# Kernel optimization log

Hardware: AMD Instinct MI355X
Metric: run time of the kernel (lower is better)

Reference implementation:

```python
import jax, jax.numpy as jnp
import numpy as np

B, D, F_UP, F_DOWN, C = 4096, 768, 12288, 12288, 256


def setup_inputs() -> dict:
    key = jax.random.key(0)
    ks = jax.random.split(key, 12)
    s = np.float32(1.0 / np.sqrt(D))
    return {
        'initial_acts': jax.random.normal(ks[0], (B, D), jnp.float32),
        'x_up': jax.random.normal(ks[1], (B, D), jnp.float32),
        'ln_scale': jax.random.uniform(ks[2], (B,), jnp.float32) + 0.5,
        'W_enc_up': jax.random.normal(ks[3], (F_UP, D), jnp.float32) * s,
        'b_enc_up': jax.random.normal(ks[4], (F_UP,), jnp.float32) * 0.01,
        'b_dec_up': jax.random.normal(ks[5], (D,), jnp.float32) * 0.01,
        'W_dec_up': jax.random.normal(ks[6], (D, F_UP), jnp.float32) * s,
        'W_enc_down': jax.random.normal(ks[7], (F_DOWN, D), jnp.float32) * s,
        'b_enc_down': jax.random.normal(ks[8], (F_DOWN,), jnp.float32) * 0.01,
        'b_dec_down': jax.random.normal(ks[9], (D,), jnp.float32) * 0.01,
        'W_dec_down': jax.random.normal(ks[10], (D, F_DOWN), jnp.float32) * s,
        'connections': jax.random.randint(ks[11], (F_DOWN, C), 0, F_UP, jnp.int64),
        'k_up': 64,
        'k_down': 64,
    }


def _topk_sparse(pre, k):
    # pre: [B, F] -> keep top-k per row, zeros elsewhere
    vals, idx = jax.lax.top_k(pre, k)
    rows = jnp.arange(pre.shape[0])[:, None]
    return jnp.zeros_like(pre).at[rows, idx].set(vals)


def _topk_encode(x, W_enc, b_enc, b_dec, k):
    # AutoEncoderTopK.encode: relu(encoder(x - b_dec)), then top-k sparsify
    pre = jax.nn.relu((x - b_dec) @ W_enc.T + b_enc)
    return _topk_sparse(pre, k)


def reference(initial_acts, x_up, ln_scale, W_enc_up, b_enc_up, b_dec_up,
              W_dec_up, W_enc_down, b_enc_down, b_dec_down, W_dec_down,
              connections, k_up, k_down):
    f_down, f_up = W_enc_down.shape[0], W_enc_up.shape[0]
    # upstream features (vanilla_forward -> features[up_name])
    feat_up = _topk_encode(x_up, W_enc_up, b_enc_up, b_dec_up, k_up)  # [B, F_up]
    # connection mask [F_down, F_up] from index tensor
    rows = jnp.arange(f_down)[:, None]
    mask = jnp.zeros((f_down, f_up), jnp.bool_).at[rows, connections].set(True)
    # get_pruned_contributions: masked virtual-weight matmul
    virtual_w = (W_enc_down @ W_dec_up) * mask                        # [F_down, F_up]
    contributions = feat_up @ virtual_w.T + (W_enc_down @ b_dec_up)   # [B, F_down]
    # get_initial_contributions + accumulate
    approx = initial_acts @ W_enc_down.T + contributions
    # layernorm scale, encoder bias, b_dec correction
    approx = approx / ln_scale[:, None] + b_enc_down - (W_enc_down @ b_dec_down)
    # downstream TopK + decode
    feat_down = _topk_sparse(approx, k_down)                          # [B, F_down]
    recon = feat_down @ W_dec_down.T + b_dec_down                     # [B, D]
    return recon
```

## Files before the change

kernel.cpp:

```cpp
#include <hip/hip_runtime.h>
#include <stdint.h>

#define B_    4096
#define D_    768
#define FUP   12288
#define FDN   12288
#define CONN  256
#define KTOP  64
#define CHUNK 1024
#define NCH   (B_ / CHUNK)
#define CH2   512
#define NCH2  (B_ / CH2)
#define PDW   1024
#define NPW   (FUP / PDW)

typedef short short8v __attribute__((ext_vector_type(8)));
typedef float f32x4  __attribute__((ext_vector_type(4)));


__device__ __forceinline__ unsigned fkey(float x) {
    unsigned u = __float_as_uint(x);
    return (u & 0x80000000u) ? ~u : (u | 0x80000000u);
}

__device__ void topk64_block(const float* vals, int n, int* gidx, float* gval,
                             unsigned* hist, int* scratch)
{
    const int tid = threadIdx.x;
    if (tid == 0) { scratch[0] = KTOP; scratch[1] = 0; scratch[2] = 0; scratch[3] = 0; }
    for (int l = 24; l >= 0; l -= 8) {
        hist[tid] = 0;
        __syncthreads();
        unsigned prefix = (unsigned)scratch[1];
        unsigned hm = (l == 24) ? 0u : (0xFFFFFFFFu << (l + 8));
        for (int i = tid; i < n; i += 256) {
            unsigned key = fkey(vals[i]);
            if ((key & hm) == (prefix & hm)) atomicAdd(&hist[(key >> l) & 255], 1u);
        }
        __syncthreads();
        if (tid == 0) {
            int need = scratch[0];
            unsigned acc = 0;
            for (int b2 = 255; b2 >= 0; --b2) {
                unsigned h = hist[b2];
                if (acc + h >= (unsigned)need) {
                    scratch[1] = (int)(prefix | ((unsigned)b2 << l));
                    scratch[0] = need - (int)acc;
                    break;
                }
                acc += h;
            }
        }
        __syncthreads();
    }
    unsigned thresh = (unsigned)scratch[1];
    for (int i = tid; i < n; i += 256) {
        float v = vals[i];
        unsigned key = fkey(v);
        if (key > thresh) {
            int p = atomicAdd(&scratch[2], 1);
            gidx[p] = i; gval[p] = v;
        } else if (key == thresh) {
            int p = atomicAdd(&scratch[3], 1);
            if (p < 64) scratch[4 + p] = i;
        }
    }
    __syncthreads();
    if (tid == 0) {
        int cnt = scratch[2];
        int ne  = KTOP - cnt;
        int ec  = scratch[3] < 64 ? scratch[3] : 64;
        for (int a2 = 0; a2 < ne; ++a2) {
            int best = 0x7fffffff, bi = -1;
            for (int q = 0; q < ec; ++q) {
                int id = scratch[4 + q];
                if (id >= 0 && id < best) { best = id; bi = q; }
            }
            if (bi >= 0) {
                scratch[4 + bi] = -1;
                gidx[cnt + a2] = best; gval[cnt + a2] = vals[best];
            }
        }
    }
    __syncthreads();
}


__global__ void k_detect(const int* __restrict__ conn, int* mode) {
    if (blockIdx.x == 0 && threadIdx.x == 0) {
        int z = 1;
        for (int i = 1; i < 128; i += 2) z &= (conn[i] == 0);
        *mode = z;
    }
}

__device__ __forceinline__ int getconn(const int* c, size_t e, int mode) {
    return mode ? c[2 * e] : c[e];
}

__global__ void k_zero(unsigned* __restrict__ p, int n) {
    for (int i = blockIdx.x * blockDim.x + threadIdx.x; i < n;
         i += gridDim.x * blockDim.x)
        p[i] = 0u;
}

__global__ void k_transpose(const float* __restrict__ in, float* __restrict__ out,
                            int R, int Cc) {
    __shared__ float t[32][33];
    int x = blockIdx.x * 32 + threadIdx.x;
    int yb = blockIdx.y * 32;
    for (int j = threadIdx.y; j < 32; j += 8)
        t[j][threadIdx.x] = in[(size_t)(yb + j) * Cc + x];
    __syncthreads();
    int xo  = yb + threadIdx.x;
    int yb2 = blockIdx.x * 32;
    for (int j = threadIdx.y; j < 32; j += 8)
        out[(size_t)(yb2 + j) * R + xo] = t[threadIdx.x][j];
}

__global__ void k_precompute(const float* __restrict__ Wup, const float* __restrict__ Wdn,
                             const float* __restrict__ b_enc_up, const float* __restrict__ b_enc_down,
                             const float* __restrict__ b_dec_up, const float* __restrict__ b_dec_down,
                             float* __restrict__ bias_up, float* __restrict__ c_in,
                             float* __restrict__ c_out) {
    int wave = threadIdx.x >> 6, lane = threadIdx.x & 63;
    int f = blockIdx.x * 4 + wave;
    if (f >= FUP) return;
    const float* ru = Wup + (size_t)f * D_;
    const float* rd = Wdn + (size_t)f * D_;
    float s1 = 0.f, s2 = 0.f, s3 = 0.f;
    for (int d = lane; d < D_; d += 64) {
        float bu = b_dec_up[d], bd = b_dec_down[d];
        s1 += ru[d] * bu;
        float w = rd[d];
        s2 += w * bu;
        s3 += w * bd;
    }
    for (int m = 32; m; m >>= 1) {
        s1 += __shfl_xor(s1, m);
        s2 += __shfl_xor(s2, m);
        s3 += __shfl_xor(s3, m);
    }
    if (!lane) {
        bias_up[f] = b_enc_up[f] - s1;
        c_in[f]  = s2;
        c_out[f] = b_enc_down[f] - s3;
    }
}

__device__ __forceinline__ unsigned short bf16rne(float f) {
    unsigned u = __float_as_uint(f);
    unsigned r = u + 0x7FFFu + ((u >> 16) & 1u);
    return (unsigned short)(r >> 16);
}
__global__ __launch_bounds__(256) void k_split3(const float* __restrict__ in,
                                                unsigned short* __restrict__ out,
                                                int R) {
    const size_t plane = (size_t)R * D_;
    size_t base = ((size_t)blockIdx.x * 256 + threadIdx.x) * 8;
    float v[8];
    *(float4*)&v[0] = *(const float4*)(in + base);
    *(float4*)&v[4] = *(const float4*)(in + base + 4);
    unsigned short h[8], m[8], l[8];
#pragma unroll
    for (int i = 0; i < 8; ++i) {
        float f = v[i];
        unsigned short hb = bf16rne(f);
        float hf = __uint_as_float((unsigned)hb << 16);
        float r1 = f - hf;
        unsigned short mb = bf16rne(r1);
        float mf = __uint_as_float((unsigned)mb << 16);
        float r2 = r1 - mf;
        unsigned short lb = bf16rne(r2);
        h[i] = hb; m[i] = mb; l[i] = lb;
    }
    *(short8v*)(out + base)             = *(short8v*)h;
    *(short8v*)(out + plane + base)     = *(short8v*)m;
    *(short8v*)(out + 2 * plane + base) = *(short8v*)l;
}

#define GBM 128
#define GBN 128
#define GBK 32

__device__ __forceinline__ void gld16(const void* g, void* l) {
    __builtin_amdgcn_global_load_lds(
        (const __attribute__((address_space(1))) unsigned int*)g,
        (__attribute__((address_space(3))) unsigned int*)l, 16, 0, 0);
}

__global__ __launch_bounds__(256, 2) void k_gemm_mfma(
    const unsigned short* __restrict__ Asp, const unsigned short* __restrict__ Bsp,
    float* __restrict__ C, const float* __restrict__ bias,
    int M, int N, int doRelu)
{
    __shared__ __attribute__((aligned(16))) unsigned short L[3072 * 8];
    const int tid = threadIdx.x;
    const int nbx = gridDim.x;
    const int nwg = nbx * gridDim.y;
    int id = blockIdx.y * nbx + blockIdx.x;
    if ((nwg & 7) == 0) id = (id & 7) * (nwg >> 3) + (id >> 3);
    const int bm = (id / nbx) * GBM, bn = (id % nbx) * GBN;

    const int wid = tid >> 6, lane = tid & 63;
    const int wm = (wid >> 1) * 64, wn = (wid & 1) * 64;
    const int l15 = lane & 15, g4 = lane >> 4;
    const size_t psA = (size_t)M * D_, psB = (size_t)N * D_;

    const unsigned short* gsrc[12];
    unsigned short* ldst[12];
#pragma unroll
    for (int q2 = 0; q2 < 12; ++q2) {
        int s  = wid * 768 + q2 * 64 + lane;
        int isB = (s >= 1536);
        int sl = isB ? (s - 1536) : s;
        int p  = sl >> 9;
        int rem = sl & 511;
        int r  = rem >> 2;
        int cs = rem & 3;
        int c  = cs ^ ((r >> 1) & 3);
        const unsigned short* bp = isB ? Bsp : Asp;
        size_t ps = isB ? psB : psA;
        int row = (isB ? bn : bm) + r;
        gsrc[q2] = bp + (size_t)p * ps + (size_t)row * D_ + c * 8;
        ldst[q2] = L + (wid * 768 + q2 * 64) * 8;
    }
    const int fA = ((wm + l15) >> 1) & 3;
    const int fB = ((wn + l15) >> 1) & 3;
    const unsigned short* aB = L + (wm + l15) * 32 + ((g4 ^ fA) * 8);
    const unsigned short* bB = L + 1536 * 8 + (wn + l15) * 32 + ((g4 ^ fB) * 8);

    f32x4 acc[4][4] = {};
    for (int k0 = 0; k0 < D_; k0 += GBK) {
        __syncthreads();
#pragma unroll
        for (int q2 = 0; q2 < 12; ++q2)
            gld16(gsrc[q2] + k0, ldst[q2]);
        __syncthreads();
        short8v af[3][4], bf[3][4];
#pragma unroll
        for (int i = 0; i < 4; ++i)
#pragma unroll
            for (int p = 0; p < 3; ++p) {
                af[p][i] = *(const short8v*)(aB + p * 4096 + i * 512);
                bf[p][i] = *(const short8v*)(bB + p * 4096 + i * 512);
            }
#pragma unroll
        for (int i = 0; i < 4; ++i)
#pragma unroll
            for (int j = 0; j < 4; ++j) {
                acc[i][j] = __builtin_amdgcn_mfma_f32_16x16x32_bf16(af[0][i], bf[0][j], acc[i][j], 0, 0, 0);
                acc[i][j] = __builtin_amdgcn_mfma_f32_16x16x32_bf16(af[0][i], bf[1][j], acc[i][j], 0, 0, 0);
                acc[i][j] = __builtin_amdgcn_mfma_f32_16x16x32_bf16(af[1][i], bf[0][j], acc[i][j], 0, 0, 0);
                acc[i][j] = __builtin_amdgcn_mfma_f32_16x16x32_bf16(af[1][i], bf[1][j], acc[i][j], 0, 0, 0);
                acc[i][j] = __builtin_amdgcn_mfma_f32_16x16x32_bf16(af[0][i], bf[2][j], acc[i][j], 0, 0, 0);
                acc[i][j] = __builtin_amdgcn_mfma_f32_16x16x32_bf16(af[2][i], bf[0][j], acc[i][j], 0, 0, 0);
            }
    }
#pragma unroll
    for (int i = 0; i < 4; ++i) {
        int gr0 = bm + wm + i * 16 + (lane >> 4) * 4;
#pragma unroll
        for (int j = 0; j < 4; ++j) {
            int gc = bn + wn + j * 16 + l15;
            float bv = bias ? bias[gc] : 0.f;
#pragma unroll
            for (int q = 0; q < 4; ++q) {
                float v = acc[i][j][q] + bv;
                if (doRelu) v = fmaxf(v, 0.f);
                C[(size_t)(gr0 + q) * N + gc] = v;
            }
        }
    }
}

__global__ __launch_bounds__(256) void k_topk_up(const float* __restrict__ big,
                                                 int* __restrict__ up_idx,
                                                 float* __restrict__ up_val) {
    __shared__ __attribute__((aligned(16))) float row[FUP];
    __shared__ unsigned hist[256];
    __shared__ int scratch[68];
    int b = blockIdx.x;
    const float4* s4 = (const float4*)(big + (size_t)b * FUP);
    float4* r4 = (float4*)row;
    for (int i = threadIdx.x; i < FUP / 4; i += 256) r4[i] = s4[i];
    __syncthreads();
    topk64_block(row, FUP, up_idx + b * 64, up_val + b * 64, hist, scratch);
}

__global__ __launch_bounds__(256) void k_sortwin(
    const int* __restrict__ conn, const int* __restrict__ mode_p,
    unsigned short* __restrict__ ent_fu, unsigned char* __restrict__ ent_c,
    unsigned short* __restrict__ woff)
{
    __shared__ int crow[CONN];
    __shared__ int cnt[NPW + 1];
    __shared__ int base[NPW + 1];
    __shared__ int cur[NPW + 1];
    int fd = blockIdx.x, tid = threadIdx.x;
    int mode = *mode_p;
    crow[tid] = getconn(conn, (size_t)fd * CONN + tid, mode);
    if (tid <= NPW) cnt[tid] = 0;
    __syncthreads();
    int fu = crow[tid];
    bool dup = false;
    for (int q = 0; q < tid; ++q) dup |= (crow[q] == fu);
    int win = dup ? NPW : (fu / PDW);
    atomicAdd(&cnt[win], 1);
    __syncthreads();
    if (tid == 0) {
        int run = 0;
        for (int i = 0; i <= NPW; ++i) { base[i] = run; run += cnt[i]; }
    }
    __syncthreads();
    if (tid <= NPW) {
        woff[fd * (NPW + 2) + tid] = (unsigned short)base[tid];
        cur[tid] = base[tid];
    }
    if (tid == 0) woff[fd * (NPW + 2) + NPW + 1] = (unsigned short)CONN;
    __syncthreads();
    int pos = atomicAdd(&cur[win], 1);
    ent_fu[(size_t)fd * CONN + pos] = (unsigned short)fu;
    ent_c[(size_t)fd * CONN + pos]  = (unsigned char)tid;
}

__global__ __launch_bounds__(256) void k_pd2(
    const float* __restrict__ Wdn, const float* __restrict__ WduT,
    const unsigned short* __restrict__ ent_fu, const unsigned char* __restrict__ ent_c,
    const unsigned short* __restrict__ woff, float* __restrict__ pd)
{
    __shared__ __attribute__((aligned(16))) float wrow[D_];
    int fd = blockIdx.x, win = blockIdx.y, tid = threadIdx.x;
    int s = woff[fd * (NPW + 2) + win];
    int e = woff[fd * (NPW + 2) + win + 1];
    if (win == NPW) {
        for (int t = s + tid; t < e; t += 256)
            pd[(size_t)fd * CONN + ent_c[(size_t)fd * CONN + t]] = 0.f;
        return;
    }
    if (s == e) return;
    const float4* wsrc = (const float4*)(Wdn + (size_t)fd * D_);
    for (int i = tid; i < D_ / 4; i += 256) ((float4*)wrow)[i] = wsrc[i];
    __syncthreads();
    const int wave = tid >> 6, lane = tid & 63;
    const int grp = lane >> 4, gi = lane & 15;
    float4 wr[12];
#pragma unroll
    for (int j = 0; j < 12; ++j)
        wr[j] = *(const float4*)&wrow[gi * 4 + j * 64];
    for (int q = s + wave * 4; q < e; q += 16) {
        int idx = q + grp;
        bool act = idx < e;
        int idxc = act ? idx : (e - 1);
        int fu = ent_fu[(size_t)fd * CONN + idxc];
        const float* wu = WduT + (size_t)fu * D_;
        float sacc = 0.f;
#pragma unroll
        for (int j = 0; j < 12; ++j) {
            float4 u = *(const float4*)&wu[gi * 4 + j * 64];
            sacc = fmaf(u.x, wr[j].x, sacc);
            sacc = fmaf(u.y, wr[j].y, sacc);
            sacc = fmaf(u.z, wr[j].z, sacc);
            sacc = fmaf(u.w, wr[j].w, sacc);
        }
#pragma unroll
        for (int m = 1; m < 16; m <<= 1) sacc += __shfl_xor(sacc, m);
        if (act && gi == 0)
            pd[(size_t)fd * CONN + ent_c[(size_t)fd * CONN + idx]] = sacc;
    }
}

__global__ void k_hist(const int* __restrict__ conn, const int* __restrict__ mode_p,
                       unsigned* __restrict__ counts, int total) {
    int mode = *mode_p;
    for (int e = blockIdx.x * blockDim.x + threadIdx.x; e < total;
         e += gridDim.x * blockDim.x)
        atomicAdd(&counts[getconn(conn, (size_t)e, mode)], 1u);
}

__global__ void k_scan(const unsigned* __restrict__ counts,
                       unsigned* __restrict__ offsets, unsigned* __restrict__ cursor) {
    __shared__ unsigned sums[256];
    int tid = threadIdx.x;
    const int CH = FUP / 256;
    unsigned local = 0;
    for (int i = 0; i < CH; ++i) local += counts[tid * CH + i];
    sums[tid] = local;
    __syncthreads();
    for (int off = 1; off < 256; off <<= 1) {
        unsigned v = 0;
        if (tid >= off) v = sums[tid - off];
        __syncthreads();
        sums[tid] += v;
        __syncthreads();
    }
    unsigned run = (tid == 0) ? 0u : sums[tid - 1];
    for (int i = 0; i < CH; ++i) {
        int idx = tid * CH + i;
        offsets[idx] = run;
        cursor[idx]  = run;
        run += counts[idx];
    }
    if (tid == 255) offsets[FUP] = run;
}

__global__ void k_scatter(const int* __restrict__ conn, const int* __restrict__ mode_p,
                          const float* __restrict__ pd, unsigned* __restrict__ cursor,
                          unsigned short* __restrict__ rev_fd, float* __restrict__ rev_w,
                          int total) {
    int mode = *mode_p;
    for (int e = blockIdx.x * blockDim.x + threadIdx.x; e < total;
         e += gridDim.x * blockDim.x) {
        int fu = getconn(conn, (size_t)e, mode);
        unsigned pos = atomicAdd(&cursor[fu], 1u);
        rev_fd[pos] = (unsigned short)(e >> 8);
        rev_w[pos]  = pd[e];
    }
}

__global__ __launch_bounds__(256) void k_down(
    const float* __restrict__ big , const float* __restrict__ ln_scale,
    const float* __restrict__ c_in, const float* __restrict__ c_out,
    const int* __restrict__ up_idx, const float* __restrict__ up_val,
    const unsigned* __restrict__ offsets, const unsigned short* __restrict__ rev_fd,
    const float* __restrict__ rev_w, int* __restrict__ down_idx,
    float* __restrict__ down_val)
{
    __shared__ __attribute__((aligned(16))) float contrib[FDN];
    __shared__ unsigned hist[256];
    __shared__ int scratch[68];
    int b = blockIdx.x, tid = threadIdx.x;
    float4* c4 = (float4*)contrib;
    for (int i = tid; i < FDN / 4; i += 256) c4[i] = make_float4(0.f, 0.f, 0.f, 0.f);
    __syncthreads();
    for (int j = 0; j < KTOP; ++j) {
        int fu = up_idx[b * 64 + j];
        float v = up_val[b * 64 + j];
        unsigned s = offsets[fu], e = offsets[fu + 1];
        for (unsigned t = s + tid; t < e; t += 256)
            atomicAdd(&contrib[rev_fd[t]], v * rev_w[t]);
    }
    __syncthreads();
    float ls = ln_scale[b];
    const float* ap = big + (size_t)b * FDN;
    for (int i = tid; i < FDN; i += 256)
        contrib[i] = (ap[i] + contrib[i] + c_in[i]) / ls + c_out[i];
    __syncthreads();
    topk64_block(contrib, FDN, down_idx + b * 64, down_val + b * 64, hist, scratch);
}

__global__ __launch_bounds__(256) void k_decode(
    const int* __restrict__ down_idx, const float* __restrict__ down_val,
    const float* __restrict__ WddT, const float* __restrict__ b_dec_down,
    float* __restrict__ out)
{
    __shared__ int fidx[64];
    __shared__ float fval[64];
    int b = blockIdx.x, tid = threadIdx.x;
    if (tid < 64) { fidx[tid] = down_idx[b * 64 + tid]; fval[tid] = down_val[b * 64 + tid]; }
    __syncthreads();
    float a0 = b_dec_down[tid], a1 = b_dec_down[tid + 256], a2 = b_dec_down[tid + 512];
    for (int j = 0; j < 64; ++j) {
        const float* r = WddT + (size_t)fidx[j] * D_;
        float v = fval[j];
        a0 += v * r[tid];
        a1 += v * r[tid + 256];
        a2 += v * r[tid + 512];
    }
    float* o = out + (size_t)b * D_;
    o[tid] = a0; o[tid + 256] = a1; o[tid + 512] = a2;
}


extern "C" void kernel_launch(void* const* d_in, const int* in_sizes, int n_in,
                              void* d_out, int out_size, void* d_ws, size_t ws_size,
                              hipStream_t stream)
{
    const float* initial_acts = (const float*)d_in[0];
    const float* x_up         = (const float*)d_in[1];
    const float* ln_scale     = (const float*)d_in[2];
    const float* W_enc_up     = (const float*)d_in[3];
    const float* b_enc_up     = (const float*)d_in[4];
    const float* b_dec_up     = (const float*)d_in[5];
    const float* W_dec_up     = (const float*)d_in[6];
    const float* W_enc_down   = (const float*)d_in[7];
    const float* b_enc_down   = (const float*)d_in[8];
    const float* b_dec_down   = (const float*)d_in[9];
    const float* W_dec_down   = (const float*)d_in[10];
    const int*   conn         = (const int*)d_in[11];
    float* out = (float*)d_out;

    char* w = (char*)d_ws;
    float*          big      = (float*)(w);
    float*          pd       = (float*)(w);
    unsigned short* ent_fu   = (unsigned short*)(w + 12582912);
    unsigned char*  ent_c    = (unsigned char*) (w + 18874368);
    unsigned short* woff     = (unsigned short*)(w + 22020096);
    unsigned short* Bsplit   = (unsigned short*)(w + 50331648);
    float*          Wt       = (float*)(w + 50331648);
    float*          rev_w    = (float*)(w + 106954752);
    unsigned short* Asplit1  = (unsigned short*)(w + 106954752);
    unsigned short* rev_fd   = (unsigned short*)(w + 119537664);
    unsigned short* Asplit2  = (unsigned short*)(w + 125829120);
    int*            up_idx   = (int*)  (w + 128188416);
    float*          up_val   = (float*)(w + 129236992);
    int*            down_idx = (int*)  (w + 130285568);
    float*          down_val = (float*)(w + 131334144);
    unsigned*       offsets  = (unsigned*)(w + 132382720);
    unsigned*       cursor   = (unsigned*)(w + 132448256);
    unsigned*       counts   = (unsigned*)(w + 132513792);
    float*          bias_up  = (float*)(w + 132579328);
    float*          c_in     = (float*)(w + 132628480);
    float*          c_out    = (float*)(w + 132677632);
    int*            mode_p   = (int*)  (w + 132726784);

    const int total_conn = FDN * CONN;
    dim3 tb(32, 8);

    k_detect<<<1, 64, 0, stream>>>(conn, mode_p);
    k_precompute<<<FUP / 4, 256, 0, stream>>>(W_enc_up, W_enc_down, b_enc_up, b_enc_down,
                                              b_dec_up, b_dec_down, bias_up, c_in, c_out);
    k_split3<<<FUP * D_ / 2048, 256, 0, stream>>>(W_enc_up, Bsplit, FUP);
    for (int c = 0; c < NCH; ++c) {
        k_split3<<<CHUNK * D_ / 2048, 256, 0, stream>>>(x_up + (size_t)c * CHUNK * D_,
                                                        Asplit1, CHUNK);
        k_gemm_mfma<<<dim3(FUP / GBN, CHUNK / GBM), 256, 0, stream>>>(
            Asplit1, Bsplit, big, bias_up, CHUNK, FUP, 1);
        k_topk_up<<<CHUNK, 256, 0, stream>>>(big, up_idx + (size_t)c * CHUNK * 64,
                                             up_val + (size_t)c * CHUNK * 64);
    }
    k_transpose<<<dim3(FUP / 32, D_ / 32), tb, 0, stream>>>(W_dec_up, Wt, D_, FUP);
    k_sortwin<<<FDN, 256, 0, stream>>>(conn, mode_p, ent_fu, ent_c, woff);
    k_pd2<<<dim3(FDN, NPW + 1), 256, 0, stream>>>(W_enc_down, Wt, ent_fu, ent_c, woff, pd);
    k_zero<<<48, 256, 0, stream>>>(counts, FUP);
    k_hist<<<4096, 256, 0, stream>>>(conn, mode_p, counts, total_conn);
    k_scan<<<1, 256, 0, stream>>>(counts, offsets, cursor);
    k_scatter<<<4096, 256, 0, stream>>>(conn, mode_p, pd, cursor, rev_fd, rev_w, total_conn);
    k_split3<<<FDN * D_ / 2048, 256, 0, stream>>>(W_enc_down, Bsplit, FDN);
    for (int c = 0; c < NCH2; ++c) {
        k_split3<<<CH2 * D_ / 2048, 256, 0, stream>>>(initial_acts + (size_t)c * CH2 * D_,
                                                      Asplit2, CH2);
        k_gemm_mfma<<<dim3(FDN / GBN, CH2 / GBM), 256, 0, stream>>>(
            Asplit2, Bsplit, big, nullptr, CH2, FDN, 0);
        k_down<<<CH2, 256, 0, stream>>>(big, ln_scale + (size_t)c * CH2, c_in, c_out,
                                        up_idx + (size_t)c * CH2 * 64,
                                        up_val + (size_t)c * CH2 * 64,
                                        offsets, rev_fd, rev_w,
                                        down_idx + (size_t)c * CH2 * 64,
                                        down_val + (size_t)c * CH2 * 64);
    }
    k_transpose<<<dim3(FDN / 32, D_ / 32), tb, 0, stream>>>(W_dec_down, Wt, D_, FDN);
    k_decode<<<B_, 256, 0, stream>>>(down_idx, down_val, Wt, b_dec_down, out);
}
```

Baseline: 3.886 ms.

## Map one 16-lane group per down-feature in masked virtual-weight kernel

The kernel that computes the pruned virtual weights now gives each 16-lane group its own downstream feature, with 16 features per block, instead of one feature per 256-thread block. Each group reads its W_enc_down row straight from global memory, so the shared-memory staging and __syncthreads go away. All 12 float4 loads of each gathered W_dec_up row are issued before the FMAs, spread over four independent accumulators, to expose more memory-level parallelism. The grid shrinks 16x and far fewer blocks exit early on empty windows. In exchange, lanes within a wave now iterate over windows of different lengths and diverge, and register pressure rises.

Result: slower. 4.042 ms (+4.0%).

```diff
diff --git a/kernel.cpp b/kernel.cpp
--- a/kernel.cpp
+++ b/kernel.cpp
@@ -324,49 +324,53 @@
     ent_c[(size_t)fd * CONN + pos]  = (unsigned char)tid;
 }
 
-__global__ __launch_bounds__(256) void k_pd2(
+__global__ __launch_bounds__(256) void k_pd5(
     const float* __restrict__ Wdn, const float* __restrict__ WduT,
     const unsigned short* __restrict__ ent_fu, const unsigned char* __restrict__ ent_c,
     const unsigned short* __restrict__ woff, float* __restrict__ pd)
 {
-    __shared__ __attribute__((aligned(16))) float wrow[D_];
-    int fd = blockIdx.x, win = blockIdx.y, tid = threadIdx.x;
-    int s = woff[fd * (NPW + 2) + win];
-    int e = woff[fd * (NPW + 2) + win + 1];
+    const int win = blockIdx.y, tid = threadIdx.x;
+    const int grp = tid >> 4, gi = tid & 15;
+    const int fd = blockIdx.x * 16 + grp;
+    const size_t ebase = (size_t)fd * CONN;
     if (win == NPW) {
-        for (int t = s + tid; t < e; t += 256)
-            pd[(size_t)fd * CONN + ent_c[(size_t)fd * CONN + t]] = 0.f;
+        int s = woff[fd * (NPW + 2) + NPW];
+        for (int t = s + gi; t < CONN; t += 16)
+            pd[ebase + ent_c[ebase + t]] = 0.f;
         return;
     }
+    const int s = woff[fd * (NPW + 2) + win];
+    const int e = woff[fd * (NPW + 2) + win + 1];
     if (s == e) return;
-    const float4* wsrc = (const float4*)(Wdn + (size_t)fd * D_);
-    for (int i = tid; i < D_ / 4; i += 256) ((float4*)wrow)[i] = wsrc[i];
-    __syncthreads();
-    const int wave = tid >> 6, lane = tid & 63;
-    const int grp = lane >> 4, gi = lane & 15;
+    const float* wd = Wdn + (size_t)fd * D_;
     float4 wr[12];
 #pragma unroll
     for (int j = 0; j < 12; ++j)
-        wr[j] = *(const float4*)&wrow[gi * 4 + j * 64];
-    for (int q = s + wave * 4; q < e; q += 16) {
-        int idx = q + grp;
-        bool act = idx < e;
-        int idxc = act ? idx : (e - 1);
-        int fu = ent_fu[(size_t)fd * CONN + idxc];
+        wr[j] = *(const float4*)(wd + gi * 4 + j * 64);
+    for (int t = s; t < e; ++t) {
+        int fu = ent_fu[ebase + t];
         const float* wu = WduT + (size_t)fu * D_;
-        float sacc = 0.f;
-#pragma unroll
-        for (int j = 0; j < 12; ++j) {
-            float4 u = *(const float4*)&wu[gi * 4 + j * 64];
-            sacc = fmaf(u.x, wr[j].x, sacc);
-            sacc = fmaf(u.y, wr[j].y, sacc);
-            sacc = fmaf(u.z, wr[j].z, sacc);
-            sacc = fmaf(u.w, wr[j].w, sacc);
+        float4 u[12];
+#pragma unroll
+        for (int j = 0; j < 12; ++j)
+            u[j] = *(const float4*)(wu + gi * 4 + j * 64);
+        float s0 = 0.f, s1 = 0.f, s2 = 0.f, s3 = 0.f;
+#pragma unroll
+        for (int j = 0; j < 12; j += 4) {
+            s0 = fmaf(u[j+0].x, wr[j+0].x, s0); s0 = fmaf(u[j+0].y, wr[j+0].y, s0);
+            s0 = fmaf(u[j+0].z, wr[j+0].z, s0); s0 = fmaf(u[j+0].w, wr[j+0].w, s0);
+            s1 = fmaf(u[j+1].x, wr[j+1].x, s1); s1 = fmaf(u[j+1].y, wr[j+1].y, s1);
+            s1 = fmaf(u[j+1].z, wr[j+1].z, s1); s1 = fmaf(u[j+1].w, wr[j+1].w, s1);
+            s2 = fmaf(u[j+2].x, wr[j+2].x, s2); s2 = fmaf(u[j+2].y, wr[j+2].y, s2);
+            s2 = fmaf(u[j+2].z, wr[j+2].z, s2); s2 = fmaf(u[j+2].w, wr[j+2].w, s2);
+            s3 = fmaf(u[j+3].x, wr[j+3].x, s3); s3 = fmaf(u[j+3].y, wr[j+3].y, s3);
+            s3 = fmaf(u[j+3].z, wr[j+3].z, s3); s3 = fmaf(u[j+3].w, wr[j+3].w, s3);
         }
+        float sacc = (s0 + s1) + (s2 + s3);
 #pragma unroll
         for (int m = 1; m < 16; m <<= 1) sacc += __shfl_xor(sacc, m);
-        if (act && gi == 0)
-            pd[(size_t)fd * CONN + ent_c[(size_t)fd * CONN + idx]] = sacc;
+        if (gi == 0)
+            pd[ebase + ent_c[ebase + t]] = sacc;
     }
 }
 
@@ -531,7 +535,8 @@
     }
     k_transpose<<<dim3(FUP / 32, D_ / 32), tb, 0, stream>>>(W_dec_up, Wt, D_, FUP);
     k_sortwin<<<FDN, 256, 0, stream>>>(conn, mode_p, ent_fu, ent_c, woff);
-    k_pd2<<<dim3(FDN, NPW + 1), 256, 0, stream>>>(W_enc_down, Wt, ent_fu, ent_c, woff, pd);
+    k_pd5<<<dim3(FDN / 16, NPW + 1), 256, 0, stream>>>(W_enc_down, Wt, ent_fu, ent_c,
+                                                       woff, pd);
     k_zero<<<48, 256, 0, stream>>>(counts, FUP);
     k_hist<<<4096, 256, 0, stream>>>(conn, mode_p, counts, total_conn);
     k_scan<<<1, 256, 0, stream>>>(counts, offsets, cursor);
```
